# Optimization experiments

Hardware: AMD Instinct MI355X
Metric: run time of the kernel (lower is better)

Reference implementation:

```python
import jax, jax.numpy as jnp
import numpy as np

B, N, D, M, H = 16, 196, 512, 20, 8


def setup_inputs() -> dict:
    key = jax.random.key(0)
    ks = jax.random.split(key, 8)
    s = 0.02  # small init scale for stable activations
    return {
        "F_clean": jax.random.normal(ks[0], (B, N, D), dtype=jnp.float32),
        "in_proj_w": jax.random.normal(ks[1], (3 * D, D), dtype=jnp.float32) * s,
        "in_proj_b": jnp.zeros((3 * D,), jnp.float32),
        "out_w": jax.random.normal(ks[2], (D, D), dtype=jnp.float32) * s,
        "out_b": jnp.zeros((D,), jnp.float32),
        "w1": jax.random.normal(ks[3], (D, D), dtype=jnp.float32) * s,
        "b1": jnp.zeros((D,), jnp.float32),
        "ln_g": jnp.ones((D,), jnp.float32),
        "ln_b": jnp.zeros((D,), jnp.float32),
        "w2": jax.random.normal(ks[4], (M, D), dtype=jnp.float32) * s,
        "b2": jnp.zeros((M,), jnp.float32),
        "templates": jax.random.normal(ks[5], (M, D), dtype=jnp.float32),
        "k": 51,  # int(D * sparsity_ratio=0.1)
    }


def reference(F_clean, in_proj_w, in_proj_b, out_w, out_b, w1, b1, ln_g, ln_b, w2, b2, templates, k):
    b, n, d = F_clean.shape
    hd = d // H
    # --- MultiheadAttention (batch_first, dropout inactive at eval) ---
    qkv = F_clean @ in_proj_w.T + in_proj_b  # [B,N,3D]
    q, kk, v = jnp.split(qkv, 3, axis=-1)
    to_heads = lambda x: x.reshape(b, n, H, hd).transpose(0, 2, 1, 3)  # [B,H,N,hd]
    q, kk, v = to_heads(q), to_heads(kk), to_heads(v)
    attn = jax.nn.softmax(jnp.einsum('bhqd,bhkd->bhqk', q, kk) / jnp.sqrt(jnp.float32(hd)), axis=-1)
    o = jnp.einsum('bhqk,bhkd->bhqd', attn, v).transpose(0, 2, 1, 3).reshape(b, n, d)
    F_enh = o @ out_w.T + out_b + F_clean  # residual
    # --- decompose MLP: Linear -> LayerNorm -> GELU(exact) -> Linear ---
    h = F_enh @ w1.T + b1
    mu = h.mean(-1, keepdims=True)
    var = h.var(-1, keepdims=True)
    h = (h - mu) / jnp.sqrt(var + 1e-5) * ln_g + ln_b
    h = jax.nn.gelu(h, approximate=False)
    Qp = h @ w2.T + b2  # [B,N,M]
    # --- outer-product expansion: [B,N,D,M] ---
    Q = F_clean[:, :, :, None] * templates.T[None, None] * Qp[:, :, None, :]
    # --- per-(b,n,m) abs-topk over D, scatter 0/1 mask, L2-normalize over D ---
    A = Q.transpose(0, 1, 3, 2)  # [B,N,M,D]
    _, idx = jax.lax.top_k(jnp.abs(A), k)
    mask = jnp.put_along_axis(jnp.zeros(A.shape, A.dtype), idx, 1.0, axis=-1, inplace=False)
    Qs = A * mask
    nrm = jnp.sqrt(jnp.sum(Qs * Qs, axis=-1, keepdims=True))
    Qn = Qs / jnp.maximum(nrm, 1e-6)  # torch F.normalize clamps norm to eps
    return Qn.transpose(0, 1, 3, 2)  # [B,N,D,M]
```

## Files before the change

### kernel.cpp

```cpp
#include <hip/hip_runtime.h>
#include <cmath>


typedef __attribute__((ext_vector_type(8))) short bf16x8v;
typedef __attribute__((ext_vector_type(4))) float f32x4v;

__device__ __forceinline__ unsigned short f2bf_rne(float x) {
  unsigned u = __float_as_uint(x);
  u += 0x7fffu + ((u >> 16) & 1u);
  return (unsigned short)(u >> 16);
}
__device__ __forceinline__ float bf2f(unsigned short h) {
  return __uint_as_float(((unsigned)h) << 16);
}
__device__ __forceinline__ void split3_1(float x,
    unsigned short& s0, unsigned short& s1, unsigned short& s2) {
  s0 = f2bf_rne(x); float r1 = x - bf2f(s0);
  s1 = f2bf_rne(r1); float r2 = r1 - bf2f(s1);
  s2 = f2bf_rne(r2);
}

__global__ __launch_bounds__(256) void prep_kernel(
    const float* __restrict__ F, unsigned short* __restrict__ Fs,
    const float* __restrict__ Wqkv, const float* __restrict__ W1,
    unsigned short* __restrict__ Walls,
    const float* __restrict__ Wo, unsigned short* __restrict__ Wcs,
    float* __restrict__ Vt,
    const float* __restrict__ bo, const float* __restrict__ b1,
    float* __restrict__ bcomb,
    const float* __restrict__ bqkv, float* __restrict__ biasAll)
{
  int b = blockIdx.x;
  int tid = threadIdx.x;

  if (b < 1296) {
    const float* X; unsigned short* O; long long i8, pstride;
    if (b < 784)       { X = F;    O = Fs;              pstride = 1605632; i8 = (long long)b * 256 + tid; }
    else if (b < 1168) { X = Wqkv; O = Walls;           pstride = 1048576; i8 = (long long)(b - 784) * 256 + tid; }
    else               { X = W1;   O = Walls + 786432;  pstride = 1048576; i8 = (long long)(b - 1168) * 256 + tid; }
    const float4 aa = *(const float4*)(X + i8 * 8);
    const float4 bb = *(const float4*)(X + i8 * 8 + 4);
    float xs[8] = {aa.x, aa.y, aa.z, aa.w, bb.x, bb.y, bb.z, bb.w};
    bf16x8v o0, o1, o2;
#pragma unroll
    for (int e = 0; e < 8; e++) {
      unsigned short s0, s1, s2;
      split3_1(xs[e], s0, s1, s2);
      o0[e] = (short)s0; o1[e] = (short)s1; o2[e] = (short)s2;
    }
    *(bf16x8v*)(O + i8 * 8)               = o0;
    *(bf16x8v*)(O + pstride + i8 * 8)     = o1;
    *(bf16x8v*)(O + 2 * pstride + i8 * 8) = o2;
    return;
  }

  if (b < 1360) {
    __shared__ __align__(16) float As[16][68];
    __shared__ __align__(16) float Bs[16][68];
    int local = b - 1296;
    int i0 = (local >> 3) * 64, j0 = (local & 7) * 64;
    int tx = tid & 15, ty = tid >> 4;
    double acc[4][4];
#pragma unroll
    for (int i = 0; i < 4; i++)
#pragma unroll
      for (int j = 0; j < 4; j++) acc[i][j] = 0.0;
    for (int k0 = 0; k0 < 512; k0 += 16) {
#pragma unroll
      for (int rr = 0; rr < 4; rr++) {
        int r = ty + 16 * rr;
        As[tx][r] = W1[(size_t)(i0 + r) * 512 + k0 + tx];
      }
      {
        int j = tid & 63, c0 = (tid >> 6) * 4;
#pragma unroll
        for (int cc = 0; cc < 4; cc++) {
          int c = c0 + cc;
          Bs[c][j] = Wo[(size_t)(k0 + c) * 512 + j0 + j];
        }
      }
      __syncthreads();
      float cf[4][4];
#pragma unroll
      for (int i = 0; i < 4; i++)
#pragma unroll
        for (int j = 0; j < 4; j++) cf[i][j] = 0.0f;
#pragma unroll
      for (int kk = 0; kk < 16; kk++) {
        float4 a4 = *(const float4*)&As[kk][ty * 4];
        float4 b4 = *(const float4*)&Bs[kk][tx * 4];
        float av[4] = {a4.x, a4.y, a4.z, a4.w};
        float bv[4] = {b4.x, b4.y, b4.z, b4.w};
#pragma unroll
        for (int i = 0; i < 4; i++)
#pragma unroll
          for (int j = 0; j < 4; j++) cf[i][j] = fmaf(av[i], bv[j], cf[i][j]);
      }
#pragma unroll
      for (int i = 0; i < 4; i++)
#pragma unroll
        for (int j = 0; j < 4; j++) acc[i][j] += (double)cf[i][j];
      __syncthreads();
    }
#pragma unroll
    for (int i = 0; i < 4; i++) {
      int gi = i0 + ty * 4 + i;
#pragma unroll
      for (int j = 0; j < 4; j++) {
        int gj = j0 + tx * 4 + j;
        float o = (float)acc[i][j];
        unsigned short l0, l1, l2;
        split3_1(o, l0, l1, l2);
        size_t idx = (size_t)gi * 512 + gj;
        Wcs[idx] = l0; Wcs[idx + 262144] = l1; Wcs[idx + 524288] = l2;
      }
    }
    return;
  }

  if (b < 1472) {
    long long p0 = (long long)(b - 1360) * 2048 + tid * 8;
#pragma unroll
    for (int e = 0; e < 8; e++) {
      long long pf = p0 + e;
      int z = (int)(pf / 1792);
      int r = (int)(pf - (long long)z * 1792);
      int d = r / 28, kk = r - d * 28;
      Vt[(size_t)z * 14336 + (size_t)d * 224 + 196 + kk] = 0.0f;
    }
    return;
  }

  if (b == 1472) {
#pragma unroll
    for (int half = 0; half < 2; half++) {
      int n = tid + half * 256;
      const float* wr = W1 + (size_t)n * 512;
      double acc = 0.0;
      for (int k = 0; k < 512; k += 4) {
        float4 wv = *(const float4*)&wr[k];
        float4 bv = *(const float4*)&bo[k];
        acc += (double)wv.x * bv.x + (double)wv.y * bv.y +
               (double)wv.z * bv.z + (double)wv.w * bv.w;
      }
      bcomb[n] = (float)(acc + (double)b1[n]);
    }
    return;
  }

#pragma unroll
  for (int e = 0; e < 8; e++) {
    int idx = tid * 8 + e;
    biasAll[idx] = (idx < 1536) ? bqkv[idx] : 0.0f;
  }
}

#define GBK 32
#define ROWB 208
#define ATILE (128 * ROWB)

__global__ __launch_bounds__(256) void gemm_ps3_kernel(
    const unsigned short* __restrict__ As, const unsigned short* __restrict__ Bs,
    float* __restrict__ C, const float* __restrict__ bias,
    const float* __restrict__ res,
    int M, int N, int ldc, int ldres,
    long long aPlane, long long bPlane,
    int kLen, long long cZStride,
    float* __restrict__ VtOut)
{
  __shared__ __align__(16) unsigned char smem[2 * ATILE];

  int z = blockIdx.z;
  int kOff = z * kLen;
  C += (size_t)z * cZStride;

  int tid = threadIdx.x;
  int lane = tid & 63, w = tid >> 6;
  int wrow = w >> 1, wcol = w & 1;
  int i0 = blockIdx.x * 128, j0 = blockIdx.y * 128;

  int r = tid >> 1, hh = tid & 1;
  int arow = i0 + r; if (arow > M - 1) arow = M - 1;
  int brow = j0 + r; if (brow > N - 1) brow = N - 1;
  const unsigned short* ap = As + (size_t)arow * 512 + hh * 16 + kOff;
  const unsigned short* bp = Bs + (size_t)brow * 512 + hh * 16 + kOff;
  unsigned swoff = (unsigned)r * ROWB + (unsigned)hh * 32;

  f32x4v acc[4][4];
#pragma unroll
  for (int fi = 0; fi < 4; fi++)
#pragma unroll
    for (int fj = 0; fj < 4; fj++) acc[fi][fj] = (f32x4v){0.f, 0.f, 0.f, 0.f};

  unsigned fr_a = (unsigned)(wrow * 64 + (lane & 15)) * ROWB + (unsigned)(lane >> 4) * 16;
  unsigned fr_b = (unsigned)(wcol * 64 + (lane & 15)) * ROWB + (unsigned)(lane >> 4) * 16 + ATILE;

  for (int k0 = 0; k0 < kLen; k0 += GBK) {
    bf16x8v a0[3], a1[3], b0v[3], b1v[3];
#pragma unroll
    for (int s = 0; s < 3; s++) {
      a0[s]  = *(const bf16x8v*)(ap + s * aPlane + k0);
      a1[s]  = *(const bf16x8v*)(ap + s * aPlane + k0 + 8);
      b0v[s] = *(const bf16x8v*)(bp + s * bPlane + k0);
      b1v[s] = *(const bf16x8v*)(bp + s * bPlane + k0 + 8);
    }
    __syncthreads();
#pragma unroll
    for (int s = 0; s < 3; s++) {
      *(bf16x8v*)(smem + swoff + s * 64)              = a0[s];
      *(bf16x8v*)(smem + swoff + s * 64 + 16)         = a1[s];
      *(bf16x8v*)(smem + ATILE + swoff + s * 64)      = b0v[s];
      *(bf16x8v*)(smem + ATILE + swoff + s * 64 + 16) = b1v[s];
    }
    __syncthreads();

    bf16x8v af[4][3];
#pragma unroll
    for (int fi = 0; fi < 4; fi++)
#pragma unroll
      for (int s = 0; s < 3; s++)
        af[fi][s] = *(const bf16x8v*)(smem + fr_a + fi * (16 * ROWB) + s * 64);

#pragma unroll
    for (int fj = 0; fj < 4; fj++) {
      bf16x8v b0 = *(const bf16x8v*)(smem + fr_b + fj * (16 * ROWB));
      bf16x8v b1 = *(const bf16x8v*)(smem + fr_b + fj * (16 * ROWB) + 64);
      bf16x8v b2 = *(const bf16x8v*)(smem + fr_b + fj * (16 * ROWB) + 128);
#pragma unroll
      for (int fi = 0; fi < 4; fi++) {
        f32x4v c = acc[fi][fj];
        c = __builtin_amdgcn_mfma_f32_16x16x32_bf16(af[fi][2], b0, c, 0, 0, 0);
        c = __builtin_amdgcn_mfma_f32_16x16x32_bf16(af[fi][1], b1, c, 0, 0, 0);
        c = __builtin_amdgcn_mfma_f32_16x16x32_bf16(af[fi][0], b2, c, 0, 0, 0);
        c = __builtin_amdgcn_mfma_f32_16x16x32_bf16(af[fi][1], b0, c, 0, 0, 0);
        c = __builtin_amdgcn_mfma_f32_16x16x32_bf16(af[fi][0], b1, c, 0, 0, 0);
        c = __builtin_amdgcn_mfma_f32_16x16x32_bf16(af[fi][0], b0, c, 0, 0, 0);
        acc[fi][fj] = c;
      }
    }
  }

#pragma unroll
  for (int fi = 0; fi < 4; fi++) {
    int row0 = i0 + wrow * 64 + fi * 16 + (lane >> 4) * 4;
#pragma unroll
    for (int fj = 0; fj < 4; fj++) {
      int col = j0 + wcol * 64 + fj * 16 + (lane & 15);
      if (col >= N) continue;
      float badd = (bias && z == 0) ? bias[col] : 0.0f;
      f32x4v v = acc[fi][fj];
#pragma unroll
      for (int rr = 0; rr < 4; rr++) {
        int row = row0 + rr;
        if (row < M) {
          float o = v[rr] + badd;
          if (res && z == 0) o += res[(size_t)row * ldres + col];
          if (VtOut && col >= 1024 && col < 1536) {
            int d = col - 1024;
            int bb = row / 196;
            int kk = row - bb * 196;
            int zz = bb * 8 + (d >> 6);
            VtOut[(size_t)zz * 14336 + (size_t)(d & 63) * 224 + kk] = o;
          } else {
            C[(size_t)row * ldc + col] = o;
          }
        }
      }
    }
  }
}

__global__ __launch_bounds__(256) void gemm_bf16x3_kernel(
    const float* __restrict__ A, const float* __restrict__ B,
    float* __restrict__ C, const float* __restrict__ bias,
    const float* __restrict__ res,
    int M, int N, int K, int lda, int ldb, int ldc,
    int zInner, long long aOuter, long long aInner,
    long long bOuter, long long bInner,
    long long cOuter, long long cInner,
    unsigned short* __restrict__ Cl, long long clPlane)
{
  int z = blockIdx.z;
  int zo = z / zInner, zi = z % zInner;
  A += zo * aOuter + zi * aInner;
  B += zo * bOuter + zi * bInner;
  long long coff = zo * cOuter + zi * cInner;
  if (C) C += coff;
  if (Cl) Cl += coff;

  __shared__ __align__(16) unsigned char smem[2 * ATILE];

  int tid = threadIdx.x;
  int lane = tid & 63, w = tid >> 6;
  int wrow = w >> 1, wcol = w & 1;
  int i0 = blockIdx.x * 128, j0 = blockIdx.y * 128;

  int srow = tid >> 1;
  int skh  = tid & 1;
  int arow = i0 + srow; if (arow > M - 1) arow = M - 1;
  int brow = j0 + srow; if (brow > N - 1) brow = N - 1;
  const float* aptr = A + (size_t)arow * lda + skh * 16;
  const float* bptr = B + (size_t)brow * ldb + skh * 16;
  unsigned swoff = (unsigned)srow * ROWB + (unsigned)skh * 32;

  f32x4v acc[4][4];
#pragma unroll
  for (int fi = 0; fi < 4; fi++)
#pragma unroll
    for (int fj = 0; fj < 4; fj++) acc[fi][fj] = (f32x4v){0.f, 0.f, 0.f, 0.f};

  unsigned fr_a = (unsigned)(wrow * 64 + (lane & 15)) * ROWB + (unsigned)(lane >> 4) * 16;
  unsigned fr_b = (unsigned)(wcol * 64 + (lane & 15)) * ROWB + (unsigned)(lane >> 4) * 16 + ATILE;

  for (int k0 = 0; k0 < K; k0 += GBK) {
    float av[16], bv[16];
    {
      const float4 q0 = *(const float4*)(aptr + k0);
      const float4 q1 = *(const float4*)(aptr + k0 + 4);
      const float4 q2 = *(const float4*)(aptr + k0 + 8);
      const float4 q3 = *(const float4*)(aptr + k0 + 12);
      av[0]=q0.x; av[1]=q0.y; av[2]=q0.z; av[3]=q0.w;
      av[4]=q1.x; av[5]=q1.y; av[6]=q1.z; av[7]=q1.w;
      av[8]=q2.x; av[9]=q2.y; av[10]=q2.z; av[11]=q2.w;
      av[12]=q3.x; av[13]=q3.y; av[14]=q3.z; av[15]=q3.w;
      const float4 r0 = *(const float4*)(bptr + k0);
      const float4 r1 = *(const float4*)(bptr + k0 + 4);
      const float4 r2 = *(const float4*)(bptr + k0 + 8);
      const float4 r3 = *(const float4*)(bptr + k0 + 12);
      bv[0]=r0.x; bv[1]=r0.y; bv[2]=r0.z; bv[3]=r0.w;
      bv[4]=r1.x; bv[5]=r1.y; bv[6]=r1.z; bv[7]=r1.w;
      bv[8]=r2.x; bv[9]=r2.y; bv[10]=r2.z; bv[11]=r2.w;
      bv[12]=r3.x; bv[13]=r3.y; bv[14]=r3.z; bv[15]=r3.w;
    }
    unsigned short ha[3][16], hb[3][16];
#pragma unroll
    for (int e = 0; e < 16; e++) {
      split3_1(av[e], ha[0][e], ha[1][e], ha[2][e]);
      split3_1(bv[e], hb[0][e], hb[1][e], hb[2][e]);
    }
    __syncthreads();
#pragma unroll
    for (int s = 0; s < 3; s++) {
      bf16x8v v0, v1, w0, w1;
#pragma unroll
      for (int e = 0; e < 8; e++) {
        v0[e] = (short)ha[s][e]; v1[e] = (short)ha[s][8 + e];
        w0[e] = (short)hb[s][e]; w1[e] = (short)hb[s][8 + e];
      }
      *(bf16x8v*)(smem + swoff + s * 64)              = v0;
      *(bf16x8v*)(smem + swoff + s * 64 + 16)         = v1;
      *(bf16x8v*)(smem + ATILE + swoff + s * 64)      = w0;
      *(bf16x8v*)(smem + ATILE + swoff + s * 64 + 16) = w1;
    }
    __syncthreads();

    bf16x8v af[4][3];
#pragma unroll
    for (int fi = 0; fi < 4; fi++)
#pragma unroll
      for (int s = 0; s < 3; s++)
        af[fi][s] = *(const bf16x8v*)(smem + fr_a + fi * (16 * ROWB) + s * 64);

#pragma unroll
    for (int fj = 0; fj < 4; fj++) {
      bf16x8v b0 = *(const bf16x8v*)(smem + fr_b + fj * (16 * ROWB));
      bf16x8v b1 = *(const bf16x8v*)(smem + fr_b + fj * (16 * ROWB) + 64);
      bf16x8v b2 = *(const bf16x8v*)(smem + fr_b + fj * (16 * ROWB) + 128);
#pragma unroll
      for (int fi = 0; fi < 4; fi++) {
        f32x4v c = acc[fi][fj];
        c = __builtin_amdgcn_mfma_f32_16x16x32_bf16(af[fi][2], b0, c, 0, 0, 0);
        c = __builtin_amdgcn_mfma_f32_16x16x32_bf16(af[fi][1], b1, c, 0, 0, 0);
        c = __builtin_amdgcn_mfma_f32_16x16x32_bf16(af[fi][0], b2, c, 0, 0, 0);
        c = __builtin_amdgcn_mfma_f32_16x16x32_bf16(af[fi][1], b0, c, 0, 0, 0);
        c = __builtin_amdgcn_mfma_f32_16x16x32_bf16(af[fi][0], b1, c, 0, 0, 0);
        c = __builtin_amdgcn_mfma_f32_16x16x32_bf16(af[fi][0], b0, c, 0, 0, 0);
        acc[fi][fj] = c;
      }
    }
  }

#pragma unroll
  for (int fi = 0; fi < 4; fi++) {
    int row0 = i0 + wrow * 64 + fi * 16 + (lane >> 4) * 4;
#pragma unroll
    for (int fj = 0; fj < 4; fj++) {
      int col = j0 + wcol * 64 + fj * 16 + (lane & 15);
      if (col >= N) continue;
      float badd = bias ? bias[col] : 0.0f;
      f32x4v v = acc[fi][fj];
#pragma unroll
      for (int rr = 0; rr < 4; rr++) {
        int row = row0 + rr;
        if (row < M) {
          float o = v[rr] + badd;
          if (res) o += res[(size_t)row * ldc + col];
          size_t idx = (size_t)row * ldc + col;
          if (Cl) {
            unsigned short l0, l1, l2;
            split3_1(o, l0, l1, l2);
            Cl[idx] = l0; Cl[idx + clPlane] = l1; Cl[idx + 2 * clPlane] = l2;
          } else {
            C[idx] = o;
          }
        }
      }
    }
  }
}

__global__ __launch_bounds__(256) void softmax_kernel(float* __restrict__ S)
{
  int row = blockIdx.x * 4 + (threadIdx.x >> 6);
  int lane = threadIdx.x & 63;
  float* sr = S + (size_t)row * 196;
  double v[4];
#pragma unroll
  for (int t = 0; t < 4; t++) {
    int j = lane + 64 * t;
    v[t] = (j < 196) ? (double)sr[j] * 0.125 : -1e300;
  }
  double mx = fmax(fmax(v[0], v[1]), fmax(v[2], v[3]));
#pragma unroll
  for (int off = 1; off < 64; off <<= 1) mx = fmax(mx, __shfl_xor(mx, off));
  double e[4]; double s = 0.0;
#pragma unroll
  for (int t = 0; t < 4; t++) {
    int j = lane + 64 * t;
    e[t] = (j < 196) ? exp(v[t] - mx) : 0.0;
    s += e[t];
  }
#pragma unroll
  for (int off = 1; off < 64; off <<= 1) s += __shfl_xor(s, off);
  double inv = 1.0 / s;
#pragma unroll
  for (int t = 0; t < 4; t++) {
    int j = lane + 64 * t;
    if (j < 196) sr[j] = (float)(e[t] * inv);
  }
}

__global__ __launch_bounds__(256) void lnw2_kernel(
    const float* __restrict__ H, const float* __restrict__ g,
    const float* __restrict__ bb, const float* __restrict__ W2,
    const float* __restrict__ B2, float* __restrict__ Qp)
{
  int row = blockIdx.x;
  const float* hr = H + (size_t)row * 512;
  int tid = threadIdx.x, lane = tid & 63, wv = tid >> 6;
  __shared__ double red[8];
  __shared__ float y[512];
  double x0 = (double)hr[tid]       + (double)hr[tid + 1605632]
            + (double)hr[tid + 3211264] + (double)hr[tid + 4816896];
  double x1 = (double)hr[tid + 256] + (double)hr[tid + 256 + 1605632]
            + (double)hr[tid + 256 + 3211264] + (double)hr[tid + 256 + 4816896];
  double s = x0 + x1;
#pragma unroll
  for (int off = 1; off < 64; off <<= 1) s += __shfl_xor(s, off);
  if (lane == 0) red[wv] = s;
  __syncthreads();
  double mu = (red[0] + red[1] + red[2] + red[3]) * (1.0 / 512.0);
  double d0 = x0 - mu, d1 = x1 - mu;
  double q = d0 * d0 + d1 * d1;
#pragma unroll
  for (int off = 1; off < 64; off <<= 1) q += __shfl_xor(q, off);
  if (lane == 0) red[4 + wv] = q;
  __syncthreads();
  double var = (red[4] + red[5] + red[6] + red[7]) * (1.0 / 512.0);
  double inv = 1.0 / sqrt(var + 1e-5);
  double y0 = d0 * inv * (double)g[tid]       + (double)bb[tid];
  double y1 = d1 * inv * (double)g[tid + 256] + (double)bb[tid + 256];
  const double ISQRT2 = 0.70710678118654752440;
  double z0 = 0.5 * y0 * (1.0 + erf(y0 * ISQRT2));
  double z1 = 0.5 * y1 * (1.0 + erf(y1 * ISQRT2));
  y[tid] = (float)z0;
  y[tid + 256] = (float)z1;
  __syncthreads();

#pragma unroll 1
  for (int t = 0; t < 5; t++) {
    int m = wv * 5 + t;
    const float* wr = W2 + (size_t)m * 512;
    double acc = 0.0;
#pragma unroll
    for (int sE = 0; sE < 8; sE++) {
      int j = lane + 64 * sE;
      acc += (double)y[j] * (double)wr[j];
    }
#pragma unroll
    for (int off = 1; off < 64; off <<= 1) acc += __shfl_xor(acc, off);
    if (lane == 0) Qp[(size_t)row * 20 + m] = (float)(acc + (double)B2[m]);
  }
}

__device__ __forceinline__ void topk_finish32(
    const unsigned* uh, const unsigned* ul, const float* apf,
    unsigned thrh, bool exact, float qp, int g,
    unsigned long long* __restrict__ masks, float* __restrict__ qif, int lane)
{
  const int KSEL = 51;
  bool sel[8];
  if (exact) {
#pragma unroll
    for (int s = 0; s < 8; s++) sel[s] = (uh[s] >= thrh);
  } else {
    int cg = 0;
#pragma unroll
    for (int s = 0; s < 8; s++) {
      sel[s] = (uh[s] > thrh);
      cg += (int)__popcll(__ballot(sel[s]));
    }
    int need = KSEL - cg;
    bool tk[8];
#pragma unroll
    for (int s = 0; s < 8; s++) tk[s] = false;
    while (need > 0) {
      unsigned long long bk = 0ULL;
#pragma unroll
      for (int s = 0; s < 8; s++) {
        if (uh[s] == thrh && !tk[s]) {
          unsigned long long key = (1ULL << 41)
                                 | ((unsigned long long)ul[s] << 9)
                                 | ((unsigned long long)(7 - s) << 6)
                                 | (unsigned long long)(63 - lane);
          bk = key > bk ? key : bk;
        }
      }
#pragma unroll
      for (int off = 1; off < 64; off <<= 1) {
        unsigned long long ob = __shfl_xor(bk, off);
        bk = ob > bk ? ob : bk;
      }
      if ((int)(63 - (bk & 63ULL)) == lane) {
        int wsI = 7 - (int)((bk >> 6) & 7ULL);
        sel[wsI] = true;
        tk[wsI] = true;
      }
      need--;
    }
  }

  float ss = 0.f;
  unsigned long long selb[8];
#pragma unroll
  for (int s = 0; s < 8; s++) {
    selb[s] = __ballot((int)sel[s]);
    if (sel[s]) ss += apf[s] * apf[s];
  }
#pragma unroll
  for (int off = 1; off < 64; off <<= 1) ss += __shfl_xor(ss, off);
  float nrm = fabsf(qp) * sqrtf(ss);
  float qid = qp / fmaxf(nrm, 1e-6f);
  if (lane == 0) {
    qif[g] = qid;
#pragma unroll
    for (int s = 0; s < 8; s++) masks[(size_t)g * 8 + s] = selb[s];
  }
}

__global__ __launch_bounds__(256) void topk_select_kernel(
    const float* __restrict__ F, const float* __restrict__ T,
    const float* __restrict__ Qp, unsigned long long* __restrict__ masks,
    float* __restrict__ qif)
{
  const int KSEL = 51;
  int wid = blockIdx.x * 4 + (threadIdx.x >> 6);
  int lane = threadIdx.x & 63;
  int g0 = wid * 2;
  int bn = g0 / 20, m0 = g0 - bn * 20;
  const float* Frow = F + (size_t)bn * 512;
  const float* T0r = T + (size_t)m0 * 512;
  const float* T1r = T0r + 512;

  unsigned uh0[8], ul0[8], uh1[8], ul1[8];
  float ap0[8], ap1[8];
#pragma unroll
  for (int s = 0; s < 8; s++) {
    double fd = (double)Frow[lane + 64 * s];
    double p0 = fd * (double)T0r[lane + 64 * s];
    double p1 = fd * (double)T1r[lane + 64 * s];
    unsigned long long u0 =
        (unsigned long long)__double_as_longlong(p0) & 0x7fffffffffffffffULL;
    unsigned long long u1 =
        (unsigned long long)__double_as_longlong(p1) & 0x7fffffffffffffffULL;
    uh0[s] = (unsigned)(u0 >> 32); ul0[s] = (unsigned)u0;
    uh1[s] = (unsigned)(u1 >> 32); ul1[s] = (unsigned)u1;
    ap0[s] = (float)fabs(p0); ap1[s] = (float)fabs(p1);
  }

  unsigned mx0 = 0u, mn0 = 0xffffffffu, mx1 = 0u, mn1 = 0xffffffffu;
#pragma unroll
  for (int s = 0; s < 8; s++) {
    mx0 = uh0[s] > mx0 ? uh0[s] : mx0;  mn0 = uh0[s] < mn0 ? uh0[s] : mn0;
    mx1 = uh1[s] > mx1 ? uh1[s] : mx1;  mn1 = uh1[s] < mn1 ? uh1[s] : mn1;
  }
#pragma unroll
  for (int off = 1; off < 64; off <<= 1) {
    unsigned a = __shfl_xor(mx0, off); mx0 = a > mx0 ? a : mx0;
    unsigned b = __shfl_xor(mn0, off); mn0 = b < mn0 ? b : mn0;
    unsigned c = __shfl_xor(mx1, off); mx1 = c > mx1 ? c : mx1;
    unsigned d = __shfl_xor(mn1, off); mn1 = d < mn1 ? d : mn1;
  }

  unsigned lo0 = mn0, hi0 = mx0 + 1u, lo1 = mn1, hi1 = mx1 + 1u;
  bool ex0 = false, ex1 = false;
  bool dn0 = (hi0 - lo0 <= 1u), dn1 = (hi1 - lo1 <= 1u);
  while (!(dn0 && dn1)) {
    if (!dn0) {
      unsigned mid = lo0 + ((hi0 - lo0) >> 1);
      int c = 0;
#pragma unroll
      for (int s = 0; s < 8; s++) c += (int)__popcll(__ballot(uh0[s] >= mid));
      if (c >= KSEL) { lo0 = mid; if (c == KSEL) { ex0 = true; dn0 = true; } }
      else hi0 = mid;
      dn0 = dn0 || (hi0 - lo0 <= 1u);
    }
    if (!dn1) {
      unsigned mid = lo1 + ((hi1 - lo1) >> 1);
      int c = 0;
#pragma unroll
      for (int s = 0; s < 8; s++) c += (int)__popcll(__ballot(uh1[s] >= mid));
      if (c >= KSEL) { lo1 = mid; if (c == KSEL) { ex1 = true; dn1 = true; } }
      else hi1 = mid;
      dn1 = dn1 || (hi1 - lo1 <= 1u);
    }
  }
  topk_finish32(uh0, ul0, ap0, lo0, ex0, Qp[g0],     g0,     masks, qif, lane);
  topk_finish32(uh1, ul1, ap1, lo1, ex1, Qp[g0 + 1], g0 + 1, masks, qif, lane);
}

__global__ __launch_bounds__(256) void topk_write_kernel(
    const float* __restrict__ F, const float* __restrict__ T,
    const unsigned long long* __restrict__ masks,
    const float* __restrict__ qif, float* __restrict__ out)
{
  int bn = blockIdx.x;
  int tid = threadIdx.x;
  __shared__ unsigned long long mw[20][8];
  __shared__ float qf[20];
  __shared__ float vt[256][21];
  if (tid < 160) ((unsigned long long*)mw)[tid] = masks[(size_t)bn * 160 + tid];
  if (tid < 20) qf[tid] = qif[(size_t)bn * 20 + tid];
  const float* Frow = F + (size_t)bn * 512;
  float* orow = out + (size_t)bn * 10240;
  __syncthreads();

#pragma unroll
  for (int half = 0; half < 2; half++) {
    int d = half * 256 + tid;
    float fd = Frow[d];
    int dw = d >> 6, db = d & 63;
#pragma unroll
    for (int m = 0; m < 20; m++) {
      bool sel = (mw[m][dw] >> db) & 1ULL;
      float tv = T[(size_t)m * 512 + d];
      vt[tid][m] = sel ? fd * tv * qf[m] : 0.0f;
    }
    __syncthreads();
#pragma unroll
    for (int k = 0; k < 5; k++) {
      int flat = (k * 256 + tid) * 4;
      float v[4];
#pragma unroll
      for (int e = 0; e < 4; e++) {
        int fe = flat + e;
        int dl = fe / 20;
        int mm = fe - dl * 20;
        v[e] = vt[dl][mm];
      }
      float4 o = {v[0], v[1], v[2], v[3]};
      *(float4*)&orow[half * 5120 + flat] = o;
    }
    __syncthreads();
  }
}

extern "C" void kernel_launch(void* const* d_in, const int* in_sizes, int n_in,
                              void* d_out, int out_size, void* d_ws, size_t ws_size,
                              hipStream_t stream) {
  const float* F    = (const float*)d_in[0];
  const float* Wqkv = (const float*)d_in[1];
  const float* bqkv = (const float*)d_in[2];
  const float* Wo   = (const float*)d_in[3];
  const float* bo   = (const float*)d_in[4];
  const float* W1   = (const float*)d_in[5];
  const float* b1   = (const float*)d_in[6];
  const float* lng  = (const float*)d_in[7];
  const float* lnb  = (const float*)d_in[8];
  const float* W2   = (const float*)d_in[9];
  const float* b2   = (const float*)d_in[10];
  const float* Tm   = (const float*)d_in[11];
  float* out = (float*)d_out;

  float* ws = (float*)d_ws;
  float* qkvw   = ws;
  float* scores = ws + 6422528;
  float* Vt     = ws + 11339776;
  float* h1p    = ws + 13174784;
  float* Qp     = ws + 19597312;
  float* bcomb  = ws + 19660032;
  float* biasAll= ws + 19660544;
  unsigned long long* masks = (unsigned long long*)(ws + 19662592);
  float* qifb   = ws + 20666112;
  unsigned short* Fs    = (unsigned short*)(ws + 20728832);
  unsigned short* Walls = (unsigned short*)(ws + 23137280);
  unsigned short* Wcs   = (unsigned short*)(ws + 24710144);
  unsigned short* Omgs  = (unsigned short*)(ws + 25103360);
  dim3 blk(256);

  prep_kernel<<<dim3(1474), blk, 0, stream>>>(
      F, Fs, Wqkv, W1, Walls, Wo, Wcs, Vt, bo, b1, bcomb, bqkv, biasAll);

  gemm_ps3_kernel<<<dim3(25, 16, 1), blk, 0, stream>>>(
      Fs, Walls, qkvw, biasAll, nullptr,
      3136, 2048, 2048, 0, 1605632LL, 1048576LL, 512, 0LL, Vt);

  gemm_bf16x3_kernel<<<dim3(2, 2, 128), blk, 0, stream>>>(
      qkvw, qkvw + 512, scores, nullptr, nullptr,
      196, 196, 64, 2048, 2048, 196,
      8, 196LL * 2048, 64, 196LL * 2048, 64, 8LL * 38416, 38416,
      nullptr, 0);

  softmax_kernel<<<dim3(6272), blk, 0, stream>>>(scores);

  gemm_bf16x3_kernel<<<dim3(2, 1, 128), blk, 0, stream>>>(
      scores, Vt, nullptr, nullptr, nullptr,
      196, 64, 196, 196, 224, 512,
      8, 8LL * 38416, 38416, 8LL * 14336, 14336, 100352, 64,
      Omgs, 1605632LL);

  gemm_ps3_kernel<<<dim3(25, 4, 4), blk, 0, stream>>>(
      Omgs, Wcs, h1p, bcomb, qkvw + 1536,
      3136, 512, 512, 2048, 1605632LL, 262144LL, 128, 1605632LL, nullptr);

  lnw2_kernel<<<dim3(3136), blk, 0, stream>>>(h1p, lng, lnb, W2, b2, Qp);

  topk_select_kernel<<<dim3(7840), blk, 0, stream>>>(F, Tm, Qp, masks, qifb);

  topk_write_kernel<<<dim3(3136), blk, 0, stream>>>(F, Tm, masks, qifb, out);
}
```

Baseline: 314.2 us.

## Prefetch GEMM tiles, swizzle XCD blocks, quaternary top-k search, split write kernel

Both bf16x3 GEMM kernels now load (and split) the next K tile into registers while the current tile's MFMAs run, hiding global-load latency at the cost of more registers. Launch bounds now request three blocks per CU. The QKV GEMM remaps block indices so neighbouring tiles land on the same XCD for better L2 reuse. Top-k threshold search tests three pivots per step (4-way) to cut the number of serial ballot rounds. The output write kernel uses one block per half row, doubling parallelism and removing a barrier.

After: 388.0 us. 1.24x slower.

```diff
diff --git a/kernel.cpp b/kernel.cpp
--- a/kernel.cpp
+++ b/kernel.cpp
@@ -159,14 +159,14 @@
 #define ROWB 208
 #define ATILE (128 * ROWB)
 
-__global__ __launch_bounds__(256) void gemm_ps3_kernel(
+__global__ __launch_bounds__(256, 3) void gemm_ps3_kernel(
     const unsigned short* __restrict__ As, const unsigned short* __restrict__ Bs,
     float* __restrict__ C, const float* __restrict__ bias,
     const float* __restrict__ res,
     int M, int N, int ldc, int ldres,
     long long aPlane, long long bPlane,
     int kLen, long long cZStride,
-    float* __restrict__ VtOut)
+    float* __restrict__ VtOut, int xcdSwz)
 {
   __shared__ __align__(16) unsigned char smem[2 * ATILE];
 
@@ -174,10 +174,19 @@
   int kOff = z * kLen;
   C += (size_t)z * cZStride;
 
+  int bx = blockIdx.x, by = blockIdx.y;
+  if (xcdSwz) {
+    int nwg = gridDim.x * gridDim.y;
+    int flat = bx + gridDim.x * by;
+    flat = (flat & 7) * (nwg >> 3) + (flat >> 3);
+    bx = flat % gridDim.x;
+    by = flat / gridDim.x;
+  }
+
   int tid = threadIdx.x;
   int lane = tid & 63, w = tid >> 6;
   int wrow = w >> 1, wcol = w & 1;
-  int i0 = blockIdx.x * 128, j0 = blockIdx.y * 128;
+  int i0 = bx * 128, j0 = by * 128;
 
   int r = tid >> 1, hh = tid & 1;
   int arow = i0 + r; if (arow > M - 1) arow = M - 1;
@@ -195,15 +204,18 @@
   unsigned fr_a = (unsigned)(wrow * 64 + (lane & 15)) * ROWB + (unsigned)(lane >> 4) * 16;
   unsigned fr_b = (unsigned)(wcol * 64 + (lane & 15)) * ROWB + (unsigned)(lane >> 4) * 16 + ATILE;
 
+  bf16x8v a0[3], a1[3], b0v[3], b1v[3];
+#define PS3_LOAD(K0)                                            \
+  _Pragma("unroll")                                             \
+  for (int s = 0; s < 3; s++) {                                 \
+    a0[s]  = *(const bf16x8v*)(ap + s * aPlane + (K0));         \
+    a1[s]  = *(const bf16x8v*)(ap + s * aPlane + (K0) + 8);     \
+    b0v[s] = *(const bf16x8v*)(bp + s * bPlane + (K0));         \
+    b1v[s] = *(const bf16x8v*)(bp + s * bPlane + (K0) + 8);     \
+  }
+
+  PS3_LOAD(0);
   for (int k0 = 0; k0 < kLen; k0 += GBK) {
-    bf16x8v a0[3], a1[3], b0v[3], b1v[3];
-#pragma unroll
-    for (int s = 0; s < 3; s++) {
-      a0[s]  = *(const bf16x8v*)(ap + s * aPlane + k0);
-      a1[s]  = *(const bf16x8v*)(ap + s * aPlane + k0 + 8);
-      b0v[s] = *(const bf16x8v*)(bp + s * bPlane + k0);
-      b1v[s] = *(const bf16x8v*)(bp + s * bPlane + k0 + 8);
-    }
     __syncthreads();
 #pragma unroll
     for (int s = 0; s < 3; s++) {
@@ -213,6 +225,8 @@
       *(bf16x8v*)(smem + ATILE + swoff + s * 64 + 16) = b1v[s];
     }
     __syncthreads();
+
+    if (k0 + GBK < kLen) { PS3_LOAD(k0 + GBK); }
 
     bf16x8v af[4][3];
 #pragma unroll
@@ -239,6 +253,7 @@
       }
     }
   }
+#undef PS3_LOAD
 
 #pragma unroll
   for (int fi = 0; fi < 4; fi++) {
@@ -270,7 +285,7 @@
   }
 }
 
-__global__ __launch_bounds__(256) void gemm_bf16x3_kernel(
+__global__ __launch_bounds__(256, 3) void gemm_bf16x3_kernel(
     const float* __restrict__ A, const float* __restrict__ B,
     float* __restrict__ C, const float* __restrict__ bias,
     const float* __restrict__ res,
@@ -312,47 +327,53 @@
   unsigned fr_a = (unsigned)(wrow * 64 + (lane & 15)) * ROWB + (unsigned)(lane >> 4) * 16;
   unsigned fr_b = (unsigned)(wcol * 64 + (lane & 15)) * ROWB + (unsigned)(lane >> 4) * 16 + ATILE;
 
+  bf16x8v pa0[3], pa1[3], pb0[3], pb1[3];
+#define BF3_LOADSPLIT(K0)                                                 \
+  { float av[16], bv[16];                                                 \
+    { const float4 q0 = *(const float4*)(aptr + (K0));                    \
+      const float4 q1 = *(const float4*)(aptr + (K0) + 4);                \
+      const float4 q2 = *(const float4*)(aptr + (K0) + 8);                \
+      const float4 q3 = *(const float4*)(aptr + (K0) + 12);               \
+      av[0]=q0.x; av[1]=q0.y; av[2]=q0.z; av[3]=q0.w;                     \
+      av[4]=q1.x; av[5]=q1.y; av[6]=q1.z; av[7]=q1.w;                     \
+      av[8]=q2.x; av[9]=q2.y; av[10]=q2.z; av[11]=q2.w;                   \
+      av[12]=q3.x; av[13]=q3.y; av[14]=q3.z; av[15]=q3.w;                 \
+      const float4 r0 = *(const float4*)(bptr + (K0));                    \
+      const float4 r1 = *(const float4*)(bptr + (K0) + 4);                \
+      const float4 r2 = *(const float4*)(bptr + (K0) + 8);                \
+      const float4 r3 = *(const float4*)(bptr + (K0) + 12);               \
+      bv[0]=r0.x; bv[1]=r0.y; bv[2]=r0.z; bv[3]=r0.w;                     \
+      bv[4]=r1.x; bv[5]=r1.y; bv[6]=r1.z; bv[7]=r1.w;                     \
+      bv[8]=r2.x; bv[9]=r2.y; bv[10]=r2.z; bv[11]=r2.w;                   \
+      bv[12]=r3.x; bv[13]=r3.y; bv[14]=r3.z; bv[15]=r3.w; }               \
+    unsigned short ha[3][16], hb[3][16];                                  \
+    _Pragma("unroll")                                                     \
+    for (int e = 0; e < 16; e++) {                                        \
+      split3_1(av[e], ha[0][e], ha[1][e], ha[2][e]);                      \
+      split3_1(bv[e], hb[0][e], hb[1][e], hb[2][e]);                      \
+    }                                                                     \
+    _Pragma("unroll")                                                     \
+    for (int s = 0; s < 3; s++) {                                         \
+      _Pragma("unroll")                                                   \
+      for (int e = 0; e < 8; e++) {                                       \
+        pa0[s][e] = (short)ha[s][e]; pa1[s][e] = (short)ha[s][8 + e];     \
+        pb0[s][e] = (short)hb[s][e]; pb1[s][e] = (short)hb[s][8 + e];     \
+      }                                                                   \
+    } }
+
+  BF3_LOADSPLIT(0);
   for (int k0 = 0; k0 < K; k0 += GBK) {
-    float av[16], bv[16];
-    {
-      const float4 q0 = *(const float4*)(aptr + k0);
-      const float4 q1 = *(const float4*)(aptr + k0 + 4);
-      const float4 q2 = *(const float4*)(aptr + k0 + 8);
-      const float4 q3 = *(const float4*)(aptr + k0 + 12);
-      av[0]=q0.x; av[1]=q0.y; av[2]=q0.z; av[3]=q0.w;
-      av[4]=q1.x; av[5]=q1.y; av[6]=q1.z; av[7]=q1.w;
-      av[8]=q2.x; av[9]=q2.y; av[10]=q2.z; av[11]=q2.w;
-      av[12]=q3.x; av[13]=q3.y; av[14]=q3.z; av[15]=q3.w;
-      const float4 r0 = *(const float4*)(bptr + k0);
-      const float4 r1 = *(const float4*)(bptr + k0 + 4);
-      const float4 r2 = *(const float4*)(bptr + k0 + 8);
-      const float4 r3 = *(const float4*)(bptr + k0 + 12);
-      bv[0]=r0.x; bv[1]=r0.y; bv[2]=r0.z; bv[3]=r0.w;
-      bv[4]=r1.x; bv[5]=r1.y; bv[6]=r1.z; bv[7]=r1.w;
-      bv[8]=r2.x; bv[9]=r2.y; bv[10]=r2.z; bv[11]=r2.w;
-      bv[12]=r3.x; bv[13]=r3.y; bv[14]=r3.z; bv[15]=r3.w;
-    }
-    unsigned short ha[3][16], hb[3][16];
-#pragma unroll
-    for (int e = 0; e < 16; e++) {
-      split3_1(av[e], ha[0][e], ha[1][e], ha[2][e]);
-      split3_1(bv[e], hb[0][e], hb[1][e], hb[2][e]);
-    }
     __syncthreads();
 #pragma unroll
     for (int s = 0; s < 3; s++) {
-      bf16x8v v0, v1, w0, w1;
-#pragma unroll
-      for (int e = 0; e < 8; e++) {
-        v0[e] = (short)ha[s][e]; v1[e] = (short)ha[s][8 + e];
-        w0[e] = (short)hb[s][e]; w1[e] = (short)hb[s][8 + e];
-      }
-      *(bf16x8v*)(smem + swoff + s * 64)              = v0;
-      *(bf16x8v*)(smem + swoff + s * 64 + 16)         = v1;
-      *(bf16x8v*)(smem + ATILE + swoff + s * 64)      = w0;
-      *(bf16x8v*)(smem + ATILE + swoff + s * 64 + 16) = w1;
+      *(bf16x8v*)(smem + swoff + s * 64)              = pa0[s];
+      *(bf16x8v*)(smem + swoff + s * 64 + 16)         = pa1[s];
+      *(bf16x8v*)(smem + ATILE + swoff + s * 64)      = pb0[s];
+      *(bf16x8v*)(smem + ATILE + swoff + s * 64 + 16) = pb1[s];
     }
     __syncthreads();
+
+    if (k0 + GBK < K) { BF3_LOADSPLIT(k0 + GBK); }
 
     bf16x8v af[4][3];
 #pragma unroll
@@ -379,6 +400,7 @@
       }
     }
   }
+#undef BF3_LOADSPLIT
 
 #pragma unroll
   for (int fi = 0; fi < 4; fi++) {
@@ -558,12 +580,33 @@
   }
 }
 
+__device__ __forceinline__ void quat_step(
+    const unsigned* uh, unsigned& lo, unsigned& hi, bool& ex, bool& dn)
+{
+  const int KSEL = 51;
+  unsigned d = hi - lo;
+  unsigned m1 = lo + (d >> 2);
+  unsigned m2 = lo + (d >> 1);
+  unsigned m3 = lo + (d - (d >> 2));
+  int c1 = 0, c2 = 0, c3 = 0;
+#pragma unroll
+  for (int s = 0; s < 8; s++) {
+    c1 += (int)__popcll(__ballot(uh[s] >= m1));
+    c2 += (int)__popcll(__ballot(uh[s] >= m2));
+    c3 += (int)__popcll(__ballot(uh[s] >= m3));
+  }
+  if (c3 >= KSEL)      { lo = m3;           if (c3 == KSEL) { ex = true; dn = true; } }
+  else if (c2 >= KSEL) { lo = m2; hi = m3;  if (c2 == KSEL) { ex = true; dn = true; } }
+  else if (c1 >= KSEL) { lo = m1; hi = m2;  if (c1 == KSEL) { ex = true; dn = true; } }
+  else                 { hi = m1; }
+  dn = dn || (hi - lo <= 1u);
+}
+
 __global__ __launch_bounds__(256) void topk_select_kernel(
     const float* __restrict__ F, const float* __restrict__ T,
     const float* __restrict__ Qp, unsigned long long* __restrict__ masks,
     float* __restrict__ qif)
 {
-  const int KSEL = 51;
   int wid = blockIdx.x * 4 + (threadIdx.x >> 6);
   int lane = threadIdx.x & 63;
   int g0 = wid * 2;
@@ -606,24 +649,8 @@
   bool ex0 = false, ex1 = false;
   bool dn0 = (hi0 - lo0 <= 1u), dn1 = (hi1 - lo1 <= 1u);
   while (!(dn0 && dn1)) {
-    if (!dn0) {
-      unsigned mid = lo0 + ((hi0 - lo0) >> 1);
-      int c = 0;
-#pragma unroll
-      for (int s = 0; s < 8; s++) c += (int)__popcll(__ballot(uh0[s] >= mid));
-      if (c >= KSEL) { lo0 = mid; if (c == KSEL) { ex0 = true; dn0 = true; } }
-      else hi0 = mid;
-      dn0 = dn0 || (hi0 - lo0 <= 1u);
-    }
-    if (!dn1) {
-      unsigned mid = lo1 + ((hi1 - lo1) >> 1);
-      int c = 0;
-#pragma unroll
-      for (int s = 0; s < 8; s++) c += (int)__popcll(__ballot(uh1[s] >= mid));
-      if (c >= KSEL) { lo1 = mid; if (c == KSEL) { ex1 = true; dn1 = true; } }
-      else hi1 = mid;
-      dn1 = dn1 || (hi1 - lo1 <= 1u);
-    }
+    if (!dn0) quat_step(uh0, lo0, hi0, ex0, dn0);
+    if (!dn1) quat_step(uh1, lo1, hi1, ex1, dn1);
   }
   topk_finish32(uh0, ul0, ap0, lo0, ex0, Qp[g0],     g0,     masks, qif, lane);
   topk_finish32(uh1, ul1, ap1, lo1, ex1, Qp[g0 + 1], g0 + 1, masks, qif, lane);
@@ -634,7 +661,8 @@
     const unsigned long long* __restrict__ masks,
     const float* __restrict__ qif, float* __restrict__ out)
 {
-  int bn = blockIdx.x;
+  int bid = blockIdx.x;
+  int bn = bid >> 1, half = bid & 1;
   int tid = threadIdx.x;
   __shared__ unsigned long long mw[20][8];
   __shared__ float qf[20];
@@ -645,33 +673,29 @@
   float* orow = out + (size_t)bn * 10240;
   __syncthreads();
 
-#pragma unroll
-  for (int half = 0; half < 2; half++) {
-    int d = half * 256 + tid;
-    float fd = Frow[d];
-    int dw = d >> 6, db = d & 63;
-#pragma unroll
-    for (int m = 0; m < 20; m++) {
-      bool sel = (mw[m][dw] >> db) & 1ULL;
-      float tv = T[(size_t)m * 512 + d];
-      vt[tid][m] = sel ? fd * tv * qf[m] : 0.0f;
-    }
-    __syncthreads();
-#pragma unroll
-    for (int k = 0; k < 5; k++) {
-      int flat = (k * 256 + tid) * 4;
-      float v[4];
-#pragma unroll
-      for (int e = 0; e < 4; e++) {
-        int fe = flat + e;
-        int dl = fe / 20;
-        int mm = fe - dl * 20;
-        v[e] = vt[dl][mm];
-      }
-      float4 o = {v[0], v[1], v[2], v[3]};
-      *(float4*)&orow[half * 5120 + flat] = o;
-    }
-    __syncthreads();
+  int d = half * 256 + tid;
+  float fd = Frow[d];
+  int dw = d >> 6, db = d & 63;
+#pragma unroll
+  for (int m = 0; m < 20; m++) {
+    bool sel = (mw[m][dw] >> db) & 1ULL;
+    float tv = T[(size_t)m * 512 + d];
+    vt[tid][m] = sel ? fd * tv * qf[m] : 0.0f;
+  }
+  __syncthreads();
+#pragma unroll
+  for (int k = 0; k < 5; k++) {
+    int flat = (k * 256 + tid) * 4;
+    float v[4];
+#pragma unroll
+    for (int e = 0; e < 4; e++) {
+      int fe = flat + e;
+      int dl = fe / 20;
+      int mm = fe - dl * 20;
+      v[e] = vt[dl][mm];
+    }
+    float4 o = {v[0], v[1], v[2], v[3]};
+    *(float4*)&orow[half * 5120 + flat] = o;
   }
 }
 
@@ -713,7 +737,7 @@
 
   gemm_ps3_kernel<<<dim3(25, 16, 1), blk, 0, stream>>>(
       Fs, Walls, qkvw, biasAll, nullptr,
-      3136, 2048, 2048, 0, 1605632LL, 1048576LL, 512, 0LL, Vt);
+      3136, 2048, 2048, 0, 1605632LL, 1048576LL, 512, 0LL, Vt, 1);
 
   gemm_bf16x3_kernel<<<dim3(2, 2, 128), blk, 0, stream>>>(
       qkvw, qkvw + 512, scores, nullptr, nullptr,
@@ -731,11 +755,11 @@
 
   gemm_ps3_kernel<<<dim3(25, 4, 4), blk, 0, stream>>>(
       Omgs, Wcs, h1p, bcomb, qkvw + 1536,
-      3136, 512, 512, 2048, 1605632LL, 262144LL, 128, 1605632LL, nullptr);
+      3136, 512, 512, 2048, 1605632LL, 262144LL, 128, 1605632LL, nullptr, 0);
 
   lnw2_kernel<<<dim3(3136), blk, 0, stream>>>(h1p, lng, lnb, W2, b2, Qp);
 
   topk_select_kernel<<<dim3(7840), blk, 0, stream>>>(F, Tm, Qp, masks, qifb);
 
-  topk_write_kernel<<<dim3(3136), blk, 0, stream>>>(F, Tm, masks, qifb, out);
-}
+  topk_write_kernel<<<dim3(6272), blk, 0, stream>>>(F, Tm, masks, qifb, out);
+}
```
